# Kernel tuning notes

Hardware: AMD Instinct MI355X
Metric: run time of the kernel (lower is better)

The kernel has to match this reference:

```python
import jax, jax.numpy as jnp
import numpy as np

EPS = 1e-6

def setup_inputs() -> dict:
    key = jax.random.key(0)
    k1, k2, k3 = jax.random.split(key, 3)
    B, D, T = 4096, 4096, 16
    inputs = jax.random.normal(k1, (B, D), dtype=jnp.float32)
    W = jax.random.normal(k2, (D, T), dtype=jnp.float32)
    W_static = jax.random.normal(k3, (D, T), dtype=jnp.float32)
    return {"inputs": inputs, "W": W, "W_static": W_static}


def _znorm(A):
    # batch z-normalization per column (population std, matching tf.math.reduce_std)
    return (A - A.mean(axis=0)) / (A.std(axis=0) + EPS)


def _pls_scan(X, Ws):
    """Sequential PLS-style deflation: factor i is produced after
    orthogonalizing X against the z-normalized previous factors."""
    B = X.shape[0]
    denom = jnp.asarray(B, X.dtype)
    T = Ws.shape[1]
    cols = [X @ Ws[:, 0:1]]  # [B,1]
    for i in range(1, T):
        C = jnp.concatenate(cols, axis=1)          # [B,i]
        conv = _znorm(C)                           # [B,i]
        beta = (conv.T @ X) / denom                # [i,D]
        lin = X - conv @ beta                      # deflated inputs [B,D]
        cols.append(lin @ Ws[:, i:i + 1])
    return jnp.concatenate(cols, axis=1)           # [B,T]


def reference(inputs, W, W_static):
    # training path of FactorLayer.call
    X = _znorm(inputs)                              # batchnorm of inputs [B,D]
    c_mat = _pls_scan(X, W_static)                  # calculate_cmat with static weights
    B = X.shape[0]
    denom = jnp.asarray(B, X.dtype)
    T = W.shape[1]
    outs = [X @ W[:, 0:1]]
    for i in range(1, T):
        Cs = c_mat[:, :i]
        conv = _znorm(Cs)
        beta = (conv.T @ X) / denom                 # [i,D]
        lin = X - conv @ beta                       # training_run output [B,D]
        outs.append(lin @ W[:, i:i + 1])
    return jnp.concatenate(outs, axis=1)            # [B,T]
```

## Files before the change

kernel.cpp:

```cpp
#include <hip/hip_runtime.h>
#include <stdint.h>


#define BB 4096
#define DD 4096
#define EPSF 1e-6f

#define O_PART    0u
#define O_GRAMM   131072u
#define O_YZ      140288u
#define O_YPART   271360u

__device__ __forceinline__ int gidx(int a, int b) {
    int lo = a < b ? a : b, hi = a < b ? b : a;
    return lo * 33 + hi;
}

__global__ __launch_bounds__(256, 2)
void kA(const float* __restrict__ in, float* __restrict__ ws) {
    __shared__ float rs[8 * 132], rq[8 * 132];
    int b = blockIdx.x, t = threadIdx.x;
    int idx = b * 256 + t;
    if (idx < 8960) ws[O_GRAMM + idx] = 0.f;
    int cg = b & 31, rg = b >> 5;
    int dbase = cg * 128, r0 = rg * 256;
    int chunk = t & 31, rr = t >> 5;
    int c0 = dbase + chunk * 4;
    float s0=0.f,s1=0.f,s2=0.f,s3=0.f,q0=0.f,q1=0.f,q2=0.f,q3=0.f;
    #pragma unroll 4
    for (int i = 0; i < 32; ++i) {
        int r = r0 + i * 8 + rr;
        float4 u = *(const float4*)&in[(size_t)r * DD + c0];
        s0 += u.x; q0 += u.x*u.x;  s1 += u.y; q1 += u.y*u.y;
        s2 += u.z; q2 += u.z*u.z;  s3 += u.w; q3 += u.w*u.w;
    }
    int lb = rr * 132 + chunk * 4;
    rs[lb+0]=s0; rs[lb+1]=s1; rs[lb+2]=s2; rs[lb+3]=s3;
    rq[lb+0]=q0; rq[lb+1]=q1; rq[lb+2]=q2; rq[lb+3]=q3;
    __syncthreads();
    float* part = ws + O_PART + (size_t)rg * 8192;
    if (t < 128) {
        float a = 0.f;
        #pragma unroll
        for (int r2 = 0; r2 < 8; ++r2) a += rs[r2 * 132 + t];
        part[dbase + t] = a;
    } else {
        int ci = t - 128;
        float a = 0.f;
        #pragma unroll
        for (int r2 = 0; r2 < 8; ++r2) a += rq[r2 * 132 + ci];
        part[4096 + dbase + ci] = a;
    }
}

__global__ __launch_bounds__(256, 8)
void kB(const float* __restrict__ in, const float* __restrict__ W,
        const float* __restrict__ Wstat, float* __restrict__ ws,
        float* __restrict__ ypart) {
    __shared__ __align__(16) float tile[64 * 33];
    __shared__ __align__(16) float inv_s[128];
    int b = blockIdx.x, t = threadIdx.x;
    int dg = b & 31, rg = b >> 5;
    int dbase = dg * 128, rowbase = rg * 64;
    int chunk = t & 7, srow = t >> 3;
    int row = t & 63;
    int jq = __builtin_amdgcn_readfirstlane(t >> 6);
    const float* inp = in + (size_t)(rowbase + srow) * DD + dbase + chunk * 4;
    float4 pf0 = *(const float4*)(inp);
    float4 pf1 = *(const float4*)(inp + (size_t)32 * DD);
    {
        if (t < 128) {
            const float* part = ws + O_PART;
            float s = 0.f, q = 0.f;
            #pragma unroll
            for (int g = 0; g < 16; ++g) {
                s += part[(size_t)g * 8192 + dbase + t];
                q += part[(size_t)g * 8192 + 4096 + dbase + t];
            }
            float m = s * (1.0f / BB);
            float var = q * (1.0f / BB) - m * m; if (var < 0.f) var = 0.f;
            inv_s[t] = 1.0f / (sqrtf(var) + EPSF);
        }
        __syncthreads();
    }
    float acc[8];
    #pragma unroll
    for (int i = 0; i < 8; ++i) acc[i] = 0.f;
    const float* wbase = (jq < 2) ? (Wstat + jq * 8) : (W + (jq - 2) * 8);
    for (int stage = 0; stage < 4; ++stage) {
        int ds0 = stage * 32;
        float4 iv4 = *(const float4*)&inv_s[ds0 + chunk * 4];
        int b0 = srow * 33 + chunk * 4;
        tile[b0 + 0] = pf0.x * iv4.x; tile[b0 + 1] = pf0.y * iv4.y;
        tile[b0 + 2] = pf0.z * iv4.z; tile[b0 + 3] = pf0.w * iv4.w;
        int b1 = (srow + 32) * 33 + chunk * 4;
        tile[b1 + 0] = pf1.x * iv4.x; tile[b1 + 1] = pf1.y * iv4.y;
        tile[b1 + 2] = pf1.z * iv4.z; tile[b1 + 3] = pf1.w * iv4.w;
        __syncthreads();
        if (stage < 3) {
            pf0 = *(const float4*)(inp + (stage + 1) * 32);
            pf1 = *(const float4*)(inp + (size_t)32 * DD + (stage + 1) * 32);
        }
        const float* trow = tile + row * 33;
        #pragma unroll 4
        for (int dl = 0; dl < 32; ++dl) {
            float xs = trow[dl];
            const float* wr = wbase + (size_t)(dbase + ds0 + dl) * 16;
            #pragma unroll
            for (int j = 0; j < 8; ++j) acc[j] += xs * wr[j];
        }
        __syncthreads();
    }
    float* dst = ypart + ((size_t)dg * BB + rowbase + row) * 32 + jq * 8;
    *(float4*)(dst + 0) = make_float4(acc[0], acc[1], acc[2], acc[3]);
    *(float4*)(dst + 4) = make_float4(acc[4], acc[5], acc[6], acc[7]);
}

__global__ __launch_bounds__(256, 2)
void kC(float* __restrict__ ws) {
    __shared__ float yz_s[8 * 34];
    int b = blockIdx.x, t = threadIdx.x;
    int rowbase = b * 8;
    int r = t >> 5, c = t & 31;
    const float* yp = ws + O_YPART;
    size_t off = (size_t)(rowbase + r) * 32 + c;
    float s = 0.f;
    #pragma unroll
    for (int dg = 0; dg < 32; ++dg) s += yp[(size_t)dg * (BB * 32) + off];
    ws[O_YZ + off] = s;
    yz_s[r * 34 + c] = s;
    if (c == 0) yz_s[r * 34 + 32] = 1.0f;
    __syncthreads();
    float* gm = ws + O_GRAMM + (size_t)(b & 7) * 1120;
    for (int p = t; p < 561; p += 256) {
        int i = 0, rem = p;
        while (rem >= 33 - i) { rem -= 33 - i; ++i; }
        int j = i + rem;
        float a2 = 0.f;
        #pragma unroll
        for (int r2 = 0; r2 < 8; ++r2) a2 += yz_s[r2 * 34 + i] * yz_s[r2 * 34 + j];
        atomicAdd(&gm[i * 33 + j], a2);
    }
}

__global__ __launch_bounds__(256, 2)
void kE(const float* __restrict__ ws, float* __restrict__ out) {
    __shared__ __align__(16) float yzs[64 * 36];
    __shared__ float Sv[33], GA[17 * 17], gz[17 * 16], v[15][17], gad[15][16],
                     gzd[15][16], gu[17], u[17], st[2], wm[17 * 16];
    int b = blockIdx.x, t = threadIdx.x;
    int rowbase = b * 64;
    const float invB = 1.0f / BB;
    const float4* src = (const float4*)(ws + O_YZ) + (size_t)rowbase * 8;
    #pragma unroll
    for (int k = 0; k < 2; ++k) {
        int idx = k * 256 + t;
        float4 f = src[idx];
        int row = idx >> 3, c4 = (idx & 7) * 4;
        yzs[row * 36 + c4 + 0] = f.x; yzs[row * 36 + c4 + 1] = f.y;
        yzs[row * 36 + c4 + 2] = f.z; yzs[row * 36 + c4 + 3] = f.w;
    }
    const float* gm = ws + O_GRAMM;
    if (t < 33) {
        float s = 0.f;
        #pragma unroll
        for (int m = 0; m < 8; ++m) s += gm[m * 1120 + gidx(t, 32)];
        Sv[t] = s;
    }
    __syncthreads();
    for (int idx = t; idx < 17 * 17; idx += 256) {
        int p = idx / 17, q = idx % 17;
        float val;
        if (p < 16 && q < 16) {
            float raw = 0.f;
            #pragma unroll
            for (int m = 0; m < 8; ++m) raw += gm[m * 1120 + gidx(p, q)];
            val = raw - Sv[p] * Sv[q] * invB;
        } else if (p == 16 && q == 16) val = (float)BB;
        else val = 0.f;
        GA[idx] = val;
    }
    for (int idx = t; idx < 17 * 16; idx += 256) {
        int p = idx / 16, tt = idx % 16;
        float val = 0.f;
        if (p < 16) {
            float raw = 0.f;
            #pragma unroll
            for (int m = 0; m < 8; ++m) raw += gm[m * 1120 + gidx(p, 16 + tt)];
            val = raw - Sv[p] * Sv[16 + tt] * invB;
        }
        gz[idx] = val;
    }
    if (t < 17) u[t] = (t == 0) ? 1.f : 0.f;
    __syncthreads();
    for (int i = 0; i < 15; ++i) {
        if (t < 17) {
            float s = 0.f;
            for (int q = 0; q < 17; ++q) s += GA[t * 17 + q] * u[q];
            gu[t] = s;
        }
        __syncthreads();
        if (t == 0) {
            float mean = gu[16] * invB, e2 = 0.f;
            for (int p = 0; p < 17; ++p) e2 += u[p] * gu[p];
            e2 *= invB;
            float var = e2 - mean * mean; if (var < 0.f) var = 0.f;
            st[0] = mean; st[1] = 1.0f / (sqrtf(var) + EPSF);
        }
        __syncthreads();
        if (t < 17) v[i][t] = (u[t] - (t == 16 ? st[0] : 0.f)) * st[1];
        __syncthreads();
        if (t < 16) {
            float s = 0.f;
            for (int p = 0; p < 17; ++p) s += v[i][p] * GA[p * 17 + t];
            gad[i][t] = s;
        } else if (t < 32) {
            int tt = t - 16;
            float s = 0.f;
            for (int p = 0; p < 17; ++p) s += v[i][p] * gz[p * 16 + tt];
            gzd[i][tt] = s;
        }
        __syncthreads();
        if (t < 17) {
            float a2 = 0.f;
            for (int j = 0; j <= i; ++j) a2 += v[j][t] * gad[j][i + 1];
            u[t] = ((t == i + 1) ? 1.f : 0.f) - a2 * invB;
        }
        __syncthreads();
    }
    for (int idx = t; idx < 17 * 16; idx += 256) {
        int p = idx / 16, tt = idx % 16;
        float s = 0.f;
        for (int j = 0; j < tt; ++j) s += v[j][p] * gzd[j][tt];
        wm[idx] = s * invB;
    }
    __syncthreads();
    if (t < 16) {
        float adj = Sv[16 + t] * invB;
        for (int p = 0; p < 16; ++p) adj -= Sv[p] * invB * wm[p * 16 + t];
        wm[16 * 16 + t] += adj;
    }
    __syncthreads();
    int row = t >> 2, c0 = (t & 3) * 4;
    const float* yr = yzs + row * 36;
    float o[4];
    #pragma unroll
    for (int k = 0; k < 4; ++k) o[k] = yr[16 + c0 + k] - wm[16 * 16 + c0 + k];
    #pragma unroll
    for (int p = 0; p < 16; ++p) {
        float yp = yr[p];
        #pragma unroll
        for (int k = 0; k < 4; ++k) o[k] -= yp * wm[p * 16 + c0 + k];
    }
    *(float4*)&out[(size_t)rowbase * 16 + t * 4] = make_float4(o[0], o[1], o[2], o[3]);
}

extern "C" void kernel_launch(void* const* d_in, const int* in_sizes, int n_in,
                              void* d_out, int out_size, void* d_ws, size_t ws_size,
                              hipStream_t stream) {
    const float* in    = (const float*)d_in[0];
    const float* W     = (const float*)d_in[1];
    const float* Wstat = (const float*)d_in[2];
    float* ws  = (float*)d_ws;
    float* out = (float*)d_out;

    kA<<<dim3(512),  dim3(256), 0, stream>>>(in, ws);
    kB<<<dim3(2048), dim3(256), 0, stream>>>(in, W, Wstat, ws, ws + O_YPART);
    kC<<<dim3(512),  dim3(256), 0, stream>>>(ws);
    kE<<<dim3(64),   dim3(256), 0, stream>>>(ws, out);
}
```

Before: 149.3 us.

## Fuse partial-sum reduction and Gram accumulation into GEMV kernel via last-block counter

Merges the separate reduction kernel kC into kB. Each block bumps a per-row-group atomic counter after a threadfence, and the last of the 32 blocks in a row group reduces the 32 partial y slices for its 64 rows. That block writes YZ and accumulates the 33x33 Gram contributions over 64 rows before issuing atomics. This removes one kernel launch and reduces the number of Gram atomics, at the cost of a serialized tail in the last block per group and a wider shared tile stride.

```diff
diff --git a/kernel.cpp b/kernel.cpp
--- a/kernel.cpp
+++ b/kernel.cpp
@@ -8,6 +8,7 @@
 
 #define O_PART    0u
 #define O_GRAMM   131072u
+#define O_CNT     140032u
 #define O_YZ      140288u
 #define O_YPART   271360u
 
@@ -21,7 +22,7 @@
     __shared__ float rs[8 * 132], rq[8 * 132];
     int b = blockIdx.x, t = threadIdx.x;
     int idx = b * 256 + t;
-    if (idx < 8960) ws[O_GRAMM + idx] = 0.f;
+    if (idx < 9024) ws[O_GRAMM + idx] = 0.f;
     int cg = b & 31, rg = b >> 5;
     int dbase = cg * 128, r0 = rg * 256;
     int chunk = t & 31, rr = t >> 5;
@@ -54,11 +55,12 @@
 }
 
 __global__ __launch_bounds__(256, 8)
-void kB(const float* __restrict__ in, const float* __restrict__ W,
-        const float* __restrict__ Wstat, float* __restrict__ ws,
-        float* __restrict__ ypart) {
-    __shared__ __align__(16) float tile[64 * 33];
+void kBC(const float* __restrict__ in, const float* __restrict__ W,
+         const float* __restrict__ Wstat, float* __restrict__ ws,
+         float* __restrict__ ypart) {
+    __shared__ __align__(16) float tile[64 * 34];
     __shared__ __align__(16) float inv_s[128];
+    __shared__ int is_last;
     int b = blockIdx.x, t = threadIdx.x;
     int dg = b & 31, rg = b >> 5;
     int dbase = dg * 128, rowbase = rg * 64;
@@ -114,31 +116,45 @@
     float* dst = ypart + ((size_t)dg * BB + rowbase + row) * 32 + jq * 8;
     *(float4*)(dst + 0) = make_float4(acc[0], acc[1], acc[2], acc[3]);
     *(float4*)(dst + 4) = make_float4(acc[4], acc[5], acc[6], acc[7]);
-}
-
-__global__ __launch_bounds__(256, 2)
-void kC(float* __restrict__ ws) {
-    __shared__ float yz_s[8 * 34];
-    int b = blockIdx.x, t = threadIdx.x;
-    int rowbase = b * 8;
-    int r = t >> 5, c = t & 31;
-    const float* yp = ws + O_YPART;
-    size_t off = (size_t)(rowbase + r) * 32 + c;
-    float s = 0.f;
-    #pragma unroll
-    for (int dg = 0; dg < 32; ++dg) s += yp[(size_t)dg * (BB * 32) + off];
-    ws[O_YZ + off] = s;
-    yz_s[r * 34 + c] = s;
-    if (c == 0) yz_s[r * 34 + 32] = 1.0f;
-    __syncthreads();
-    float* gm = ws + O_GRAMM + (size_t)(b & 7) * 1120;
+
+    __threadfence();
+    __syncthreads();
+    if (t == 0) {
+        unsigned int* cnt = (unsigned int*)(ws + O_CNT);
+        is_last = (atomicAdd(&cnt[rg], 1u) == 31u);
+    }
+    __syncthreads();
+    if (!is_last) return;
+    __threadfence();
+
+    float* yz_s = tile;
+    #pragma unroll
+    for (int k = 0; k < 2; ++k) {
+        int idx = k * 256 + t;
+        int r = idx >> 3, q = (idx & 7) * 4;
+        size_t off = (size_t)(rowbase + r) * 32 + q;
+        float x0=0.f, x1=0.f, x2=0.f, x3=0.f;
+        #pragma unroll 8
+        for (int dg2 = 0; dg2 < 32; ++dg2) {
+            float4 v = *(const float4*)&ypart[(size_t)dg2 * (BB * 32) + off];
+            x0 += v.x; x1 += v.y; x2 += v.z; x3 += v.w;
+        }
+        *(float4*)&ws[O_YZ + off] = make_float4(x0, x1, x2, x3);
+        int lbase = r * 34 + q;
+        yz_s[lbase + 0] = x0; yz_s[lbase + 1] = x1;
+        yz_s[lbase + 2] = x2; yz_s[lbase + 3] = x3;
+        if (q == 0) yz_s[r * 34 + 32] = 1.0f;
+    }
+    __syncthreads();
+    float* gm = ws + O_GRAMM + (size_t)(rg & 7) * 1120;
     for (int p = t; p < 561; p += 256) {
         int i = 0, rem = p;
         while (rem >= 33 - i) { rem -= 33 - i; ++i; }
         int j = i + rem;
         float a2 = 0.f;
-        #pragma unroll
-        for (int r2 = 0; r2 < 8; ++r2) a2 += yz_s[r2 * 34 + i] * yz_s[r2 * 34 + j];
+        #pragma unroll 8
+        for (int r2 = 0; r2 < 64; ++r2)
+            a2 += yz_s[r2 * 34 + i] * yz_s[r2 * 34 + j];
         atomicAdd(&gm[i * 33 + j], a2);
     }
 }
@@ -265,7 +281,6 @@
     float* out = (float*)d_out;
 
     kA<<<dim3(512),  dim3(256), 0, stream>>>(in, ws);
-    kB<<<dim3(2048), dim3(256), 0, stream>>>(in, W, Wstat, ws, ws + O_YPART);
-    kC<<<dim3(512),  dim3(256), 0, stream>>>(ws);
+    kBC<<<dim3(2048), dim3(256), 0, stream>>>(in, W, Wstat, ws, ws + O_YPART);
     kE<<<dim3(64),   dim3(256), 0, stream>>>(ws, out);
 }
```

After: 462.3 us. 3.1x slower.
